# Performance work log

Hardware: AMD Instinct MI355X
Metric: run time of the kernel (lower is better)

## Reference

```python
import jax, jax.numpy as jnp
import numpy as np

B, N, C, H = 4, 2048, 1024, 16
HD = C // H
SCALE = HD ** -0.5


def setup_inputs() -> dict:
    key = jax.random.key(0)
    k1, k2, k3, k4 = jax.random.split(key, 4)
    x = jax.random.normal(k1, (B, N, C), dtype=jnp.float32)
    # torch nn.Linear weights: [out, in]
    w_qkv = jax.random.normal(k2, (3 * C, C), dtype=jnp.float32) * (C ** -0.5)
    w_proj = jax.random.normal(k3, (C, C), dtype=jnp.float32) * (C ** -0.5)
    b_proj = jax.random.normal(k4, (C,), dtype=jnp.float32) * 0.01
    return {"x": x, "w_qkv": w_qkv, "w_proj": w_proj, "b_proj": b_proj}


def reference(x, w_qkv, w_proj, b_proj):
    Bx, Nx, Cx = x.shape
    # qkv projection: [B,N,3C] -> [3,B,H,N,HD]
    qkv = jnp.einsum('bnc,dc->bnd', x, w_qkv)
    qkv = qkv.reshape(Bx, Nx, 3, H, HD).transpose(2, 0, 3, 1, 4)
    q, k, v = qkv[0], qkv[1], qkv[2]
    attn = jnp.einsum('bhqd,bhkd->bhqk', q, k) * SCALE
    attn = jax.nn.softmax(attn, axis=-1)
    # dropout p=0.0 (eval/identity)
    out = jnp.einsum('bhqk,bhkd->bhqd', attn, v)
    out = out.transpose(0, 2, 1, 3).reshape(Bx, Nx, Cx)
    return jnp.einsum('bnc,dc->bnd', out, w_proj) + b_proj
```

## Files before the change

### kernel.cpp

```cpp
#include <hip/hip_runtime.h>


typedef float f32x2 __attribute__((ext_vector_type(2)));
typedef float f32x4 __attribute__((ext_vector_type(4)));
typedef float f32x16 __attribute__((ext_vector_type(16)));
typedef __bf16 bf16x8 __attribute__((ext_vector_type(8)));
typedef __bf16 bf16x4 __attribute__((ext_vector_type(4)));
typedef __bf16 bf16x2 __attribute__((ext_vector_type(2)));
typedef unsigned int u32;
typedef unsigned int u32x2 __attribute__((ext_vector_type(2)));

__device__ __forceinline__ void async16(const void* g, void* l) {
  __builtin_amdgcn_global_load_lds((const __attribute__((address_space(1))) unsigned int*)g,
                                   (__attribute__((address_space(3))) unsigned int*)l, 16, 0, 0);
}
__device__ __forceinline__ u32 cvtpk_bf16(float lo, float hi) {
  u32 r;
  asm("v_cvt_pk_bf16_f32 %0, %1, %2" : "=v"(r) : "v"(lo), "v"(hi));
  return r;
}
__device__ __forceinline__ void swap32(u32& a, u32& b) {
  asm volatile("v_permlane32_swap_b32 %0, %1" : "+v"(a), "+v"(b));
}
__device__ __forceinline__ float xmax64(float x) { return fmaxf(x, __shfl_xor(x, 32, 64)); }
__device__ __forceinline__ float exp2v(float x) { return __builtin_amdgcn_exp2f(x); }
__device__ __forceinline__ f32x2 pkmax(f32x2 a, f32x2 b) {
  return f32x2{ fmaxf(a.x, b.x), fmaxf(a.y, b.y) };
}

__global__ __launch_bounds__(256) void cast_to_bf16(const float* __restrict__ x,
                                                    const float* __restrict__ wq,
                                                    const float* __restrict__ wp,
                                                    __bf16* __restrict__ xo,
                                                    __bf16* __restrict__ wqo,
                                                    __bf16* __restrict__ wpo) {
  long i = (long)blockIdx.x * 256 + threadIdx.x;
  const float* s; __bf16* d; long j;
  if (i < 2097152L)      { s = x;  d = xo;  j = i; }
  else if (i < 2883584L) { s = wq; d = wqo; j = i - 2097152L; }
  else                   { s = wp; d = wpo; j = i - 2883584L; }
  float4 v = ((const float4*)s)[j];
  bf16x4 o = { (__bf16)v.x, (__bf16)v.y, (__bf16)v.z, (__bf16)v.w };
  ((bf16x4*)d)[j] = o;
}

template <int EPI>
__global__ __launch_bounds__(256) void gemm_bt(const __bf16* __restrict__ A,
                                               const __bf16* __restrict__ Bw,
                                               __bf16* __restrict__ Oq,
                                               float* __restrict__ Of,
                                               const float* __restrict__ bias) {
  const int tid = threadIdx.x;
  const int lane = tid & 63, w = tid >> 6;
  const int arow = lane & 15, agrp = lane >> 4;
  const int wm = w >> 1, wn = w & 1;
  const int bm = blockIdx.x, bn = blockIdx.y;
  __shared__ __bf16 As[128 * 32];
  __shared__ __bf16 Bs[128 * 32];
  f32x4 acc[4][4] = {};

  const int c0 = tid, c1 = tid + 256;
  const __bf16* Ag0 = A + ((size_t)(bm * 128 + (c0 >> 2)) << 10) + (c0 & 3) * 8;
  const __bf16* Ag1 = A + ((size_t)(bm * 128 + (c1 >> 2)) << 10) + (c1 & 3) * 8;
  const __bf16* Bg0 = Bw + ((size_t)(bn * 128 + (c0 >> 2)) << 10) + (c0 & 3) * 8;
  const __bf16* Bg1 = Bw + ((size_t)(bn * 128 + (c1 >> 2)) << 10) + (c1 & 3) * 8;

  for (int kt = 0; kt < 1024; kt += 32) {
    async16(Ag0 + kt, &As[c0 * 8]);
    async16(Ag1 + kt, &As[c1 * 8]);
    async16(Bg0 + kt, &Bs[c0 * 8]);
    async16(Bg1 + kt, &Bs[c1 * 8]);
    __syncthreads();
    bf16x8 af[4], bfr[4];
#pragma unroll
    for (int mi = 0; mi < 4; ++mi)
      af[mi] = *(const bf16x8*)&As[(wm * 64 + mi * 16 + arow) * 32 + agrp * 8];
#pragma unroll
    for (int ni = 0; ni < 4; ++ni)
      bfr[ni] = *(const bf16x8*)&Bs[(wn * 64 + ni * 16 + arow) * 32 + agrp * 8];
#pragma unroll
    for (int mi = 0; mi < 4; ++mi)
#pragma unroll
      for (int ni = 0; ni < 4; ++ni)
        acc[mi][ni] = __builtin_amdgcn_mfma_f32_16x16x32_bf16(af[mi], bfr[ni], acc[mi][ni], 0, 0, 0);
    __syncthreads();
  }

  const int rowb = bm * 128 + wm * 64 + agrp * 4;
  const int colb = bn * 128 + wn * 64 + arow;
  if (EPI == 0) {
#pragma unroll
    for (int mi = 0; mi < 4; ++mi) {
      const int row = rowb + mi * 16;
      const int bidx = row >> 11;
#pragma unroll
      for (int ni = 0; ni < 4; ++ni) {
        f32x4 v = acc[mi][ni];
        const int col = colb + ni * 16;
        const int which = col >> 10;
        const int h = (col >> 6) & 15;
        const int hd = col & 63;
        const float s = (which == 0) ? 0.18033688011112042f : 1.0f;
        __bf16* dst = Oq + ((size_t)which * 64 + bidx * 16 + h) * (size_t)(2048 * 64) + hd;
#pragma unroll
        for (int i = 0; i < 4; ++i)
          dst[(size_t)((row + i) & 2047) * 64] = (__bf16)(v[i] * s);
      }
    }
  } else {
#pragma unroll
    for (int mi = 0; mi < 4; ++mi) {
      const int row = rowb + mi * 16;
#pragma unroll
      for (int ni = 0; ni < 4; ++ni) {
        const int col = colb + ni * 16;
        const float bv = bias[col];
        f32x4 v = acc[mi][ni];
#pragma unroll
        for (int i = 0; i < 4; ++i)
          Of[(size_t)(row + i) * 1024 + col] = v[i] + bv;
      }
    }
  }
}

__global__ __launch_bounds__(256) void mhsa_attn(const __bf16* __restrict__ QKV,
                                                 __bf16* __restrict__ Out) {
  const int tid = threadIdx.x;
  const int lane = tid & 63, w = tid >> 6;
  const int blk = blockIdx.x;
  const int bh = blk & 63, qt = blk >> 6;
  const int lq = lane & 31, hi = lane >> 5;
  const int l7 = lane & 7, l3 = lane >> 3;

  const size_t bhoff = (size_t)bh * (2048 * 64);
  const __bf16* Qp = QKV + bhoff;
  const __bf16* Kp = QKV + (size_t)(64 * 2048 * 64) + bhoff;
  const __bf16* Vp = QKV + (size_t)(128 * 2048 * 64) + bhoff;

  __shared__ char smem[32768];

  const int q0 = qt * 128 + w * 32;

  bf16x8 qf[4];
#pragma unroll
  for (int s = 0; s < 4; ++s)
    qf[s] = *(const bf16x8*)&Qp[(size_t)(q0 + lq) * 64 + s * 16 + hi * 8];

  union { u32 wv[4]; bf16x8 v; } ou;
  ou.wv[0] = ou.wv[1] = ou.wv[2] = ou.wv[3] = 0x3F803F80u;
  const bf16x8 onesA = ou.v;

  f32x16 Oacc0 = 0.f, Oacc1 = 0.f;
  f32x16 lacc = 0.f;
  float m_run = -1e30f;

  const __bf16* Kg = Kp + (size_t)(w * 16 + l3) * 64 + ((l7 ^ l3) * 8);
  const int kldoff = w * 2048 + lane * 16;

  const int c8v = tid >> 5, k0v = (tid & 31) * 2;

  {
    async16(Kg, smem + kldoff);
    async16(Kg + 512, smem + kldoff + 1024);
    bf16x8 v0 = *(const bf16x8*)&Vp[(size_t)k0v * 64 + c8v * 8];
    bf16x8 v1 = *(const bf16x8*)&Vp[(size_t)(k0v + 1) * 64 + c8v * 8];
    char* Vb = smem + 8192;
#pragma unroll
    for (int j = 0; j < 8; ++j) {
      const int d = c8v * 8 + j;
      bf16x2 pr = { v0[j], v1[j] };
      *(bf16x2*)(Vb + ((d * 128 + k0v * 2) ^ ((d & 7) << 4))) = pr;
    }
  }
  __syncthreads();

  for (int t = 0; t < 32; ++t) {
    char* Kc = smem + (t & 1) * 16384;
    char* Vc = Kc + 8192;
    char* Kn = smem + ((t & 1) ^ 1) * 16384;
    char* Vn = Kn + 8192;

    bf16x8 v0n, v1n;
    const bool pf = (t < 31);
    if (pf) {
      const size_t ktn = (size_t)(t + 1) * 64;
      async16(Kg + ktn * 64, Kn + kldoff);
      async16(Kg + ktn * 64 + 512, Kn + kldoff + 1024);
      v0n = *(const bf16x8*)&Vp[(ktn + k0v) * 64 + c8v * 8];
      v1n = *(const bf16x8*)&Vp[(ktn + k0v + 1) * 64 + c8v * 8];
    }

    f32x16 st0 = 0.f, st1 = 0.f;
    __builtin_amdgcn_s_setprio(1);
#pragma unroll
    for (int s = 0; s < 4; ++s) {
      bf16x8 kf = *(const bf16x8*)(Kc + lq * 128 + ((s * 32 + hi * 16) ^ (l7 << 4)));
      st0 = __builtin_amdgcn_mfma_f32_32x32x16_bf16(kf, qf[s], st0, 0, 0, 0);
    }
#pragma unroll
    for (int s = 0; s < 4; ++s) {
      bf16x8 kf = *(const bf16x8*)(Kc + (32 + lq) * 128 + ((s * 32 + hi * 16) ^ (l7 << 4)));
      st1 = __builtin_amdgcn_mfma_f32_32x32x16_bf16(kf, qf[s], st1, 0, 0, 0);
    }
    __builtin_amdgcn_s_setprio(0);

    f32x2 m2 = f32x2{ st0[0], st0[1] };
#pragma unroll
    for (int r = 1; r < 8; ++r) m2 = pkmax(m2, f32x2{ st0[2 * r], st0[2 * r + 1] });
#pragma unroll
    for (int r = 0; r < 8; ++r) m2 = pkmax(m2, f32x2{ st1[2 * r], st1[2 * r + 1] });
    float mx = xmax64(fmaxf(m2.x, m2.y));

    if (!__all(mx - m_run <= 8.f)) {
      const float mnew = fmaxf(m_run, mx);
      const float fs = exp2v(m_run - mnew);
      m_run = mnew;
#pragma unroll
      for (int r = 0; r < 16; ++r) { Oacc0[r] *= fs; Oacc1[r] *= fs; lacc[r] *= fs; }
    }

    const float mb = m_run;
#pragma unroll
    for (int r = 0; r < 16; ++r) st0[r] = exp2v(st0[r] - mb);
#pragma unroll
    for (int r = 0; r < 16; ++r) st1[r] = exp2v(st1[r] - mb);

    bf16x8 pa[4];
#pragma unroll
    for (int kb = 0; kb < 2; ++kb) {
      const f32x16& st = kb ? st1 : st0;
#pragma unroll
      for (int s16 = 0; s16 < 2; ++s16) {
        u32 A0 = cvtpk_bf16(st[8 * s16 + 0], st[8 * s16 + 1]);
        u32 B0 = cvtpk_bf16(st[8 * s16 + 4], st[8 * s16 + 5]);
        swap32(A0, B0);
        u32 A1 = cvtpk_bf16(st[8 * s16 + 2], st[8 * s16 + 3]);
        u32 B1 = cvtpk_bf16(st[8 * s16 + 6], st[8 * s16 + 7]);
        swap32(A1, B1);
        union { u32 wv[4]; bf16x8 v; } uu;
        uu.wv[0] = A0; uu.wv[1] = A1; uu.wv[2] = B0; uu.wv[3] = B1;
        pa[kb * 2 + s16] = uu.v;
      }
    }

    __builtin_amdgcn_s_setprio(1);
#pragma unroll
    for (int ks = 0; ks < 4; ++ks) {
      bf16x8 vf = *(const bf16x8*)(Vc + lq * 128 + ((ks * 32 + hi * 16) ^ (l7 << 4)));
      Oacc0 = __builtin_amdgcn_mfma_f32_32x32x16_bf16(vf, pa[ks], Oacc0, 0, 0, 0);
      lacc = __builtin_amdgcn_mfma_f32_32x32x16_bf16(onesA, pa[ks], lacc, 0, 0, 0);
    }
#pragma unroll
    for (int ks = 0; ks < 4; ++ks) {
      bf16x8 vf = *(const bf16x8*)(Vc + (32 + lq) * 128 + ((ks * 32 + hi * 16) ^ (l7 << 4)));
      Oacc1 = __builtin_amdgcn_mfma_f32_32x32x16_bf16(vf, pa[ks], Oacc1, 0, 0, 0);
    }
    __builtin_amdgcn_s_setprio(0);

    if (pf) {
#pragma unroll
      for (int j = 0; j < 8; ++j) {
        const int d = c8v * 8 + j;
        bf16x2 pr = { v0n[j], v1n[j] };
        *(bf16x2*)(Vn + ((d * 128 + k0v * 2) ^ ((d & 7) << 4))) = pr;
      }
    }
    __syncthreads();
  }

  const float inv = 1.0f / lacc[0];
  const int b = bh >> 4, h = bh & 15;
  __bf16* orow = Out + ((size_t)(b * 2048 + q0 + lq)) * 1024 + h * 64;
#pragma unroll
  for (int db = 0; db < 2; ++db) {
    const f32x16& O = db ? Oacc1 : Oacc0;
#pragma unroll
    for (int rg = 0; rg < 4; ++rg) {
      u32 plo = cvtpk_bf16(O[rg * 4 + 0] * inv, O[rg * 4 + 1] * inv);
      u32 phi = cvtpk_bf16(O[rg * 4 + 2] * inv, O[rg * 4 + 3] * inv);
      u32x2 pk = { plo, phi };
      *(u32x2*)&orow[db * 32 + rg * 8 + hi * 4] = pk;
    }
  }
}

extern "C" void kernel_launch(void* const* d_in, const int* in_sizes, int n_in,
                              void* d_out, int out_size, void* d_ws, size_t ws_size,
                              hipStream_t stream) {
  const float* x  = (const float*)d_in[0];
  const float* wq = (const float*)d_in[1];
  const float* wp = (const float*)d_in[2];
  const float* bp = (const float*)d_in[3];
  char* ws = (char*)d_ws;

  __bf16* xo   = (__bf16*)(ws);
  __bf16* wqo  = (__bf16*)(ws + 16777216);
  __bf16* wpo  = (__bf16*)(ws + 23068672);
  __bf16* qkv  = (__bf16*)(ws + 25165824);
  __bf16* aout = xo;
  float* y = (float*)d_out;

  cast_to_bf16<<<12288, 256, 0, stream>>>(x, wq, wp, xo, wqo, wpo);
  gemm_bt<0><<<dim3(64, 24), 256, 0, stream>>>(xo, wqo, qkv, nullptr, nullptr);
  mhsa_attn<<<1024, 256, 0, stream>>>(qkv, aout);
  gemm_bt<1><<<dim3(64, 8), 256, 0, stream>>>(aout, wpo, nullptr, y, bp);
}
```

Before: 203.3 us.

## Add 4-stage async LDS pipeline to bf16 projection GEMM

Replaces the single-buffered GEMM main loop with a four-slot LDS ring buffer filled by async global-to-LDS loads issued three stages ahead. Per-iteration synchronization becomes a partial vmcnt wait plus barrier, so global load latency overlaps MFMA work. It also raises wave priority around the MFMA block. LDS use grows to 64 KB per block, which may reduce occupancy. The last iterations issue wrapped redundant loads, and the slot reuse ordering relies on the barrier placement.

```diff
diff --git a/kernel.cpp b/kernel.cpp
--- a/kernel.cpp
+++ b/kernel.cpp
@@ -55,8 +55,7 @@
   const int arow = lane & 15, agrp = lane >> 4;
   const int wm = w >> 1, wn = w & 1;
   const int bm = blockIdx.x, bn = blockIdx.y;
-  __shared__ __bf16 As[128 * 32];
-  __shared__ __bf16 Bs[128 * 32];
+  __shared__ char gsm[65536];
   f32x4 acc[4][4] = {};
 
   const int c0 = tid, c1 = tid + 256;
@@ -65,26 +64,42 @@
   const __bf16* Bg0 = Bw + ((size_t)(bn * 128 + (c0 >> 2)) << 10) + (c0 & 3) * 8;
   const __bf16* Bg1 = Bw + ((size_t)(bn * 128 + (c1 >> 2)) << 10) + (c1 & 3) * 8;
 
-  for (int kt = 0; kt < 1024; kt += 32) {
-    async16(Ag0 + kt, &As[c0 * 8]);
-    async16(Ag1 + kt, &As[c1 * 8]);
-    async16(Bg0 + kt, &Bs[c0 * 8]);
-    async16(Bg1 + kt, &Bs[c1 * 8]);
-    __syncthreads();
+#define GSTAGE(slot, kt)                                    \
+  {                                                         \
+    char* S_ = gsm + (slot) * 16384;                        \
+    async16(Ag0 + (kt), S_ + c0 * 16);                      \
+    async16(Ag1 + (kt), S_ + c1 * 16);                      \
+    async16(Bg0 + (kt), S_ + 8192 + c0 * 16);               \
+    async16(Bg1 + (kt), S_ + 8192 + c1 * 16);               \
+  }
+
+  GSTAGE(0, 0)
+  GSTAGE(1, 32)
+  GSTAGE(2, 64)
+  asm volatile("s_waitcnt vmcnt(8)" ::: "memory");
+  __builtin_amdgcn_s_barrier();
+
+  for (int t = 0; t < 32; ++t) {
+    GSTAGE((t + 3) & 3, ((t + 3) & 31) * 32)
+    char* S = gsm + (t & 3) * 16384;
     bf16x8 af[4], bfr[4];
 #pragma unroll
     for (int mi = 0; mi < 4; ++mi)
-      af[mi] = *(const bf16x8*)&As[(wm * 64 + mi * 16 + arow) * 32 + agrp * 8];
+      af[mi] = *(const bf16x8*)(S + ((wm * 64 + mi * 16 + arow) * 32 + agrp * 8) * 2);
 #pragma unroll
     for (int ni = 0; ni < 4; ++ni)
-      bfr[ni] = *(const bf16x8*)&Bs[(wn * 64 + ni * 16 + arow) * 32 + agrp * 8];
+      bfr[ni] = *(const bf16x8*)(S + 8192 + ((wn * 64 + ni * 16 + arow) * 32 + agrp * 8) * 2);
+    __builtin_amdgcn_s_setprio(1);
 #pragma unroll
     for (int mi = 0; mi < 4; ++mi)
 #pragma unroll
       for (int ni = 0; ni < 4; ++ni)
         acc[mi][ni] = __builtin_amdgcn_mfma_f32_16x16x32_bf16(af[mi], bfr[ni], acc[mi][ni], 0, 0, 0);
-    __syncthreads();
-  }
+    __builtin_amdgcn_s_setprio(0);
+    asm volatile("s_waitcnt vmcnt(8)" ::: "memory");
+    __builtin_amdgcn_s_barrier();
+  }
+#undef GSTAGE
 
   const int rowb = bm * 128 + wm * 64 + agrp * 4;
   const int colb = bn * 128 + wn * 64 + arow;
```

Result: slower. 207.8 us (+2.2%).

## Double GEMM K-tile to 64 with XOR-swizzled LDS layout and MFMA priority

Applied to the files above, without the earlier changes.

Raises the GEMM K step per iteration from 32 to 64, which halves the number of barrier pairs. The LDS tiles now hold 128-byte rows with an XOR swizzle on the 16-byte chunks, so the fragment reads avoid bank conflicts. Wave priority is raised around the MFMA block. LDS use doubles to 32 KB per block, which may lower occupancy, and there is still no double buffering.

```diff
diff --git a/kernel.cpp b/kernel.cpp
--- a/kernel.cpp
+++ b/kernel.cpp
@@ -55,34 +55,42 @@
   const int arow = lane & 15, agrp = lane >> 4;
   const int wm = w >> 1, wn = w & 1;
   const int bm = blockIdx.x, bn = blockIdx.y;
-  __shared__ __bf16 As[128 * 32];
-  __shared__ __bf16 Bs[128 * 32];
+  __shared__ char gsm[32768];
+  char* AsB = gsm;
+  char* BsB = gsm + 16384;
   f32x4 acc[4][4] = {};
 
-  const int c0 = tid, c1 = tid + 256;
-  const __bf16* Ag0 = A + ((size_t)(bm * 128 + (c0 >> 2)) << 10) + (c0 & 3) * 8;
-  const __bf16* Ag1 = A + ((size_t)(bm * 128 + (c1 >> 2)) << 10) + (c1 & 3) * 8;
-  const __bf16* Bg0 = Bw + ((size_t)(bn * 128 + (c0 >> 2)) << 10) + (c0 & 3) * 8;
-  const __bf16* Bg1 = Bw + ((size_t)(bn * 128 + (c1 >> 2)) << 10) + (c1 & 3) * 8;
-
-  for (int kt = 0; kt < 1024; kt += 32) {
-    async16(Ag0 + kt, &As[c0 * 8]);
-    async16(Ag1 + kt, &As[c1 * 8]);
-    async16(Bg0 + kt, &Bs[c0 * 8]);
-    async16(Bg1 + kt, &Bs[c1 * 8]);
+  const int row0 = tid >> 3, cc0 = tid & 7;
+  const int sc0 = cc0 ^ (row0 & 7);
+  const __bf16* Ag = A + ((size_t)(bm * 128 + row0) << 10) + sc0 * 8;
+  const __bf16* Bg = Bw + ((size_t)(bn * 128 + row0) << 10) + sc0 * 8;
+  const int ld0 = tid * 16;
+
+  for (int kt = 0; kt < 1024; kt += 64) {
+#pragma unroll
+    for (int k = 0; k < 4; ++k) {
+      async16(Ag + kt + (size_t)k * 32768, AsB + ld0 + k * 4096);
+      async16(Bg + kt + (size_t)k * 32768, BsB + ld0 + k * 4096);
+    }
     __syncthreads();
-    bf16x8 af[4], bfr[4];
-#pragma unroll
-    for (int mi = 0; mi < 4; ++mi)
-      af[mi] = *(const bf16x8*)&As[(wm * 64 + mi * 16 + arow) * 32 + agrp * 8];
-#pragma unroll
-    for (int ni = 0; ni < 4; ++ni)
-      bfr[ni] = *(const bf16x8*)&Bs[(wn * 64 + ni * 16 + arow) * 32 + agrp * 8];
-#pragma unroll
-    for (int mi = 0; mi < 4; ++mi)
+#pragma unroll
+    for (int kk = 0; kk < 2; ++kk) {
+      bf16x8 af[4], bfr[4];
+      const int csw = (kk * 64 + agrp * 16) ^ ((arow & 7) << 4);
+#pragma unroll
+      for (int mi = 0; mi < 4; ++mi)
+        af[mi] = *(const bf16x8*)(AsB + (wm * 64 + mi * 16 + arow) * 128 + csw);
 #pragma unroll
       for (int ni = 0; ni < 4; ++ni)
-        acc[mi][ni] = __builtin_amdgcn_mfma_f32_16x16x32_bf16(af[mi], bfr[ni], acc[mi][ni], 0, 0, 0);
+        bfr[ni] = *(const bf16x8*)(BsB + (wn * 64 + ni * 16 + arow) * 128 + csw);
+      __builtin_amdgcn_s_setprio(1);
+#pragma unroll
+      for (int mi = 0; mi < 4; ++mi)
+#pragma unroll
+        for (int ni = 0; ni < 4; ++ni)
+          acc[mi][ni] = __builtin_amdgcn_mfma_f32_16x16x32_bf16(af[mi], bfr[ni], acc[mi][ni], 0, 0, 0);
+      __builtin_amdgcn_s_setprio(0);
+    }
     __syncthreads();
   }
 
```

New measurement: 192.9 us. -5.1%, faster.
